# Optimization experiments

Hardware: AMD Instinct MI355X
Metric: run time of the kernel (lower is better)

The kernel has to match this reference:

```python
import jax, jax.numpy as jnp
import numpy as np

DIM = 64          # RefineNet dim
MDIM = 32         # EGNN m_dim
NLAY = 16         # 4 refine stages x n_layer=4 EGNN layers
VOCAB = 26        # len(RNAAlphabet)
PAD = 1           # padding_idx
NPOS = 4096 + PAD + 1
N = 23            # atoms per residue (hard-coded repeat(1,1,23))
EIN = 2 * DIM + 1 # edge MLP input dim

silu = jax.nn.silu

def _lin(x, w, b):
    return x @ w + b

def _egnn(feats, coors, p):
    ew1, eb1, ew2, eb2, cw1, cb1, cw2, cb2, nw1, nb1, nw2, nb2, g, beta = p
    B, Nn, D = feats.shape
    rel = coors[:, :, None, :] - coors[:, None, :, :]            # [B,Nn,Nn,3]
    dist = jnp.sum(rel * rel, -1, keepdims=True)                 # [B,Nn,Nn,1]
    fi = jnp.broadcast_to(feats[:, :, None, :], (B, Nn, Nn, D))
    fj = jnp.broadcast_to(feats[:, None, :, :], (B, Nn, Nn, D))
    edge_in = jnp.concatenate([fi, fj, dist], -1)                # [B,Nn,Nn,2D+1]
    m_ij = silu(_lin(silu(_lin(edge_in, ew1, eb1)), ew2, eb2))   # [B,Nn,Nn,MDIM]
    w = _lin(silu(_lin(m_ij, cw1, cb1)), cw2, cb2)[..., 0]       # [B,Nn,Nn]
    nrm = jnp.sqrt(dist)
    normed = rel / jnp.maximum(nrm, 1e-8)
    # CoorsNorm uses LayerNorm over a size-1 dim: (x - mean) == 0, so phase == beta
    phase = g * jnp.zeros_like(nrm) + beta
    coors_out = jnp.einsum('bij,bijc->bic', w * (1.0 / 50.0), phase * normed) + coors
    m_i = m_ij.sum(-2)
    node_out = _lin(silu(_lin(jnp.concatenate([feats, m_i], -1), nw1, nb1)), nw2, nb2) + feats
    return node_out, coors_out

def _forward(tokens, cords, tok_emb, pos_emb, ew1, eb1, ew2, eb2,
             cw1, cb1, cw2, cb2, nw1, nb1, nw2, nb2, ln_g, ln_b):
    stacked = (ew1, eb1, ew2, eb2, cw1, cb1, cw2, cb2, nw1, nb1, nw2, nb2, ln_g, ln_b)
    t = tokens[:, 0, :]                                  # [b,l]
    b, l = t.shape
    tok = jnp.broadcast_to(t[:, :, None], (b, l, N))     # repeat(1,1,23)
    fea = tok_emb[tok]                                   # [b,l,N,DIM]
    mask = (tok.reshape(b * l, N) != PAD).astype(jnp.int32)
    pos = jnp.cumsum(mask, axis=1) * mask + PAD
    fea = fea + pos_emb[pos].reshape(fea.shape)
    co = cords.reshape(b, l, N, 3)

    def run(f, c, start):
        for k in range(4):
            p = tuple(a[start + k] for a in stacked)
            f, c = _egnn(f, c, p)
        return f, c

    f, c = run(fea.reshape(b * l, N, DIM), co.reshape(b * l, N, 3), 0)
    f = jnp.swapaxes(f.reshape(b, l, N, DIM), 1, 2)
    c = jnp.swapaxes(c.reshape(b, l, N, 3), 1, 2)
    f, c = run(f.reshape(b * N, l, DIM), c.reshape(b * N, l, 3), 4)
    f = jnp.swapaxes(f.reshape(b, N, l, DIM), 1, 2)
    c = jnp.swapaxes(c.reshape(b, N, l, 3), 1, 2)
    f, c = run(f.reshape(b * l, N, DIM), c.reshape(b * l, N, 3), 8)
    f = jnp.swapaxes(f.reshape(b, l, N, DIM), 1, 2)
    c = jnp.swapaxes(c.reshape(b, l, N, 3), 1, 2)
    f, c = run(f.reshape(b * N, l, DIM), c.reshape(b * N, l, 3), 12)
    c = jnp.swapaxes(c.reshape(b, N, l, 3), 1, 2)
    return c.reshape(b, l * N, 3)

def setup_inputs():
    key = jax.random.key(0)
    ks = jax.random.split(key, 20)
    b, l = 2, 96
    s = 0.02
    def W(k, shp):
        return jax.random.normal(k, shp, jnp.float32) * s
    return {
        "tokens": jax.random.randint(ks[0], (b, 1, l), 0, VOCAB),
        "cords": jax.random.normal(ks[1], (b, l * N, 3), jnp.float32),
        "tok_emb": W(ks[2], (VOCAB, DIM)),
        "pos_emb": W(ks[3], (NPOS, DIM)).at[PAD].set(0.0),
        "ew1": W(ks[4], (NLAY, EIN, EIN * 2)), "eb1": W(ks[5], (NLAY, EIN * 2)),
        "ew2": W(ks[6], (NLAY, EIN * 2, MDIM)), "eb2": W(ks[7], (NLAY, MDIM)),
        "cw1": W(ks[8], (NLAY, MDIM, MDIM * 4)), "cb1": W(ks[9], (NLAY, MDIM * 4)),
        "cw2": W(ks[10], (NLAY, MDIM * 4, 1)), "cb2": W(ks[11], (NLAY, 1)),
        "nw1": W(ks[12], (NLAY, DIM + MDIM, DIM * 2)), "nb1": W(ks[13], (NLAY, DIM * 2)),
        "nw2": W(ks[14], (NLAY, DIM * 2, DIM)), "nb2": W(ks[15], (NLAY, DIM)),
        "ln_g": 1.0 + W(ks[16], (NLAY, 1)),
        "ln_b": W(ks[17], (NLAY, 1)),
    }

def reference(tokens, cords, tok_emb, pos_emb, ew1, eb1, ew2, eb2,
              cw1, cb1, cw2, cb2, nw1, nb1, nw2, nb2, ln_g, ln_b):
    return _forward(tokens, cords, tok_emb, pos_emb, ew1, eb1, ew2, eb2,
                    cw1, cb1, cw2, cb2, nw1, nb1, nw2, nb2, ln_g, ln_b)
```

## Files before the change

### kernel.cpp

```cpp
#include <hip/hip_runtime.h>
#include <math.h>

#define DIM   64
#define MDIM  32
#define NLAY  16
#define PAD   1
#define NB    2
#define LL    96
#define NN    23
#define NNODE (NB*LL*NN)
#define EIN   129
#define EH    258
#define KP    272
#define NK0   17
#define NH    128
#define BPITCH 276
#define APITCH 274
#define NOUT  516
#define NTILE 17
#define XP    104
#define HP    136
#define OP    560

typedef __attribute__((ext_vector_type(8)))  short        bf16x8;
typedef __attribute__((ext_vector_type(16))) float        f32x16;
typedef __attribute__((ext_vector_type(4)))  unsigned int uint4v;

__device__ __forceinline__ float silu_f(float x) {
    float e = __expf(-x);
    return x * __builtin_amdgcn_rcpf(1.0f + e);
}
__device__ __forceinline__ unsigned short bf16_rn(float x) {
    unsigned u = __float_as_uint(x);
    u += 0x7FFF + ((u >> 16) & 1);
    return (unsigned short)(u >> 16);
}
__device__ __forceinline__ float bf16_up(unsigned short h) {
    return __uint_as_float(((unsigned)h) << 16);
}
__device__ __forceinline__ int fwd_map(int nf, int alongL) {
    if (alongL) {
        int b = nf / (LL * NN);
        int rem = nf % (LL * NN);
        int l = rem / NN, n = rem % NN;
        return (b * NN + n) * LL + l;
    }
    return nf;
}
__device__ __forceinline__ int inv_map(int gnode, int alongL) {
    if (alongL) {
        int g = gnode / LL, l = gnode % LL;
        int b = g / NN, n = g % NN;
        return (b * LL + l) * NN + n;
    }
    return gnode;
}

__global__ void k_embed(const int* __restrict__ tokens,
                        const float* __restrict__ tok_emb,
                        const float* __restrict__ pos_emb,
                        float* __restrict__ feats) {
    int idx = blockIdx.x * blockDim.x + threadIdx.x;
    if (idx < NNODE * DIM) {
        int node = idx / DIM, d = idx % DIM;
        int b = node / (LL * NN);
        int rem = node % (LL * NN);
        int n = rem % NN;
        int l = rem / NN;
        int t = tokens[b * LL + l];
        float f = tok_emb[t * DIM + d];
        if (t != PAD) f += pos_emb[(n + 2) * DIM + d];
        feats[idx] = f;
    }
}

__global__ void k_prep(const float* __restrict__ ew1, const float* __restrict__ ew2,
                       const float* __restrict__ cw1, const float* __restrict__ cb1,
                       const float* __restrict__ cw2,
                       const float* __restrict__ nw1, const float* __restrict__ nw2,
                       float* __restrict__ wdF, unsigned short* __restrict__ ew2P,
                       unsigned short* __restrict__ cw1P,
                       float* __restrict__ cb1P, float* __restrict__ cw2P,
                       unsigned short* __restrict__ ew1P,
                       unsigned short* __restrict__ nw1P,
                       unsigned short* __restrict__ nw2P) {
    int idx = blockIdx.x * blockDim.x + threadIdx.x;
    if (idx < NLAY * KP) {
        int L = idx / KP, k = idx % KP;
        float v = (k < EH) ? ew1[(size_t)L * EIN * EH + 128 * EH + k] : 0.0f;
        wdF[idx] = bf16_up(bf16_rn(v));
    }
    if (idx < NLAY * NK0 * 512) {
        int L = idx / (NK0 * 512); int r = idx % (NK0 * 512);
        int k0 = r / 512; int r2 = r % 512;
        int lane = r2 >> 3, j = r2 & 7;
        int k = k0 * 16 + (lane >> 5) * 8 + j;
        int n = lane & 31;
        float v = (k < EH) ? ew2[((size_t)L * EH + k) * MDIM + n] : 0.0f;
        ew2P[idx] = bf16_rn(v);
    }
    if (idx < NLAY * 4096) {
        int L = idx / 4096; int r = idx % 4096;
        int mb = r / 1024; int r2 = r % 1024;
        int k0 = r2 / 512; int r3 = r2 % 512;
        int lane = r3 >> 3, j = r3 & 7;
        int k = k0 * 16 + (lane >> 5) * 8 + j;
        int o = mb * 32 + (lane & 31);
        cw1P[idx] = bf16_rn(cw1[((size_t)L * MDIM + k) * NH + o]);
    }
    if (idx < NLAY * 128) {
        int L = idx / 128; int r = idx % 128;
        int hlf = r / 64; int r2 = r % 64;
        int mb = r2 / 16, reg = r2 % 16;
        int o = mb * 32 + (reg & 3) + 8 * (reg >> 2) + 4 * hlf;
        cb1P[idx] = cb1[L * NH + o];
        cw2P[idx] = cw2[L * NH + o];
    }
    if (idx < NLAY * NTILE * 4 * 512) {
        int L = idx / (NTILE * 4 * 512); int r = idx % (NTILE * 4 * 512);
        int nt = r / 2048; int r2 = r % 2048;
        int ks = r2 / 512; int r3 = r2 % 512;
        int lane = r3 >> 3, j = r3 & 7;
        int d = ks * 16 + (lane >> 5) * 8 + j;
        int o = nt * 32 + (lane & 31);
        float v = 0.0f;
        if (o < EH)        v = ew1[(size_t)L * EIN * EH + d * EH + o];
        else if (o < NOUT) v = ew1[(size_t)L * EIN * EH + (DIM + d) * EH + (o - EH)];
        ew1P[idx] = bf16_rn(v);
    }
    if (idx < NLAY * 4 * 6 * 512) {
        int L = idx / 12288; int r = idx % 12288;
        int nt = r / 3072; int r2 = r % 3072;
        int ks = r2 / 512; int r3 = r2 % 512;
        int lane = r3 >> 3, j = r3 & 7;
        int k = ks * 16 + (lane >> 5) * 8 + j;
        int n = nt * 32 + (lane & 31);
        nw1P[idx] = bf16_rn(nw1[((size_t)L * (DIM + MDIM) + k) * NH + n]);
    }
    if (idx < NLAY * 2 * 8 * 512) {
        int L = idx / 8192; int r = idx % 8192;
        int nt = r / 4096; int r2 = r % 4096;
        int ks = r2 / 512; int r3 = r2 % 512;
        int lane = r3 >> 3, j = r3 & 7;
        int k = ks * 16 + (lane >> 5) * 8 + j;
        int n = nt * 32 + (lane & 31);
        nw2P[idx] = bf16_rn(nw2[((size_t)L * NH + k) * DIM + n]);
    }
}

__global__ __launch_bounds__(256)
void k_np(const float* __restrict__ fIn, const float* __restrict__ coSrc,
          const float* __restrict__ miL, const float* __restrict__ dL,
          const unsigned short* __restrict__ nw1PL, const float* __restrict__ nb1L,
          const unsigned short* __restrict__ nw2PL, const float* __restrict__ nb2L,
          const unsigned short* __restrict__ ew1PL, const float* __restrict__ eb1L,
          float* __restrict__ fOut, float* __restrict__ coDst,
          float* __restrict__ miNext, float* __restrict__ dNext,
          unsigned short* __restrict__ aH, unsigned short* __restrict__ bH,
          int aL0, int aL1, int doNode) {
    __shared__ unsigned short xS[32 * XP];
    __shared__ unsigned short hS[32 * HP];
    __shared__ unsigned short outS[32 * OP];
    __shared__ int gsrcS[32], gdstS[32];

    int n0  = blockIdx.x * 32;
    int tid = threadIdx.x;
    int wave = tid >> 6, lane = tid & 63, half = lane >> 5, e = lane & 31;

    if (tid < 32) {
        gsrcS[tid] = fwd_map(n0 + tid, aL0);
        gdstS[tid] = fwd_map(n0 + tid, aL1);
    }
    __syncthreads();

    for (int i = 0; i < 8; i++) {
        int x = tid + 256 * i;
        int node = x >> 6, d = x & 63;
        xS[node * XP + d] = bf16_rn(fIn[(n0 + node) * DIM + d]);
    }
    if (doNode) {
        for (int i = 0; i < 4; i++) {
            int x = tid + 256 * i;
            int node = x >> 5, d = x & 31;
            xS[node * XP + DIM + d] = bf16_rn(miL[(size_t)gsrcS[node] * MDIM + d]);
        }
    }
    for (int x = tid; x < 32 * 14; x += 256) {
        int node = x / 14, c = EH + x % 14;
        outS[node * OP + c] = 0;
    }
    if (tid < 96) {
        int node = tid / 3, c = tid % 3;
        int gs = gsrcS[node], gd = gdstS[node];
        float cv = coSrc[gs * 3 + c] + (doNode ? dL[gs * 3 + c] : 0.0f);
        coDst[gd * 3 + c] = cv;
        dNext[gd * 3 + c] = 0.0f;
    }
    for (int i = 0; i < 4; i++) {
        int x = tid + 256 * i;
        int node = x >> 5, d = x & 31;
        miNext[(size_t)gdstS[node] * MDIM + d] = 0.0f;
    }
    __syncthreads();

    if (doNode) {
        {
            int nt = wave;
            f32x16 acc;
#pragma unroll
            for (int q = 0; q < 16; q++) acc[q] = 0.0f;
#pragma unroll
            for (int ks = 0; ks < 6; ks++) {
                uint4v au = *(const uint4v*)(xS + e * XP + ks * 16 + half * 8);
                uint4v bu = *(const uint4v*)(nw1PL + ((size_t)(nt * 6 + ks) * 512 + lane * 8));
                acc = __builtin_amdgcn_mfma_f32_32x32x16_bf16(
                          __builtin_bit_cast(bf16x8, au),
                          __builtin_bit_cast(bf16x8, bu), acc, 0, 0, 0);
            }
            int o = nt * 32 + e;
            float b1 = nb1L[o];
#pragma unroll
            for (int q = 0; q < 16; q++) {
                int row = (q & 3) + 8 * (q >> 2) + 4 * half;
                hS[row * HP + o] = bf16_rn(silu_f(acc[q] + b1));
            }
        }
        __syncthreads();

        if (wave < 2) {
            int nt = wave;
            f32x16 acc;
#pragma unroll
            for (int q = 0; q < 16; q++) acc[q] = 0.0f;
#pragma unroll
            for (int ks = 0; ks < 8; ks++) {
                uint4v au = *(const uint4v*)(hS + e * HP + ks * 16 + half * 8);
                uint4v bu = *(const uint4v*)(nw2PL + ((size_t)(nt * 8 + ks) * 512 + lane * 8));
                acc = __builtin_amdgcn_mfma_f32_32x32x16_bf16(
                          __builtin_bit_cast(bf16x8, au),
                          __builtin_bit_cast(bf16x8, bu), acc, 0, 0, 0);
            }
            int o = nt * 32 + e;
            float b2 = nb2L[o];
#pragma unroll
            for (int q = 0; q < 16; q++) {
                int row = (q & 3) + 8 * (q >> 2) + 4 * half;
                float fo = acc[q] + b2 + bf16_up(xS[row * XP + o]);
                fOut[(size_t)(n0 + row) * DIM + o] = fo;
                xS[row * XP + o] = bf16_rn(fo);
            }
        }
        __syncthreads();
    }

    {
        uint4v afrag[4];
#pragma unroll
        for (int ks = 0; ks < 4; ks++)
            afrag[ks] = *(const uint4v*)(xS + e * XP + ks * 16 + half * 8);

        for (int nt = wave; nt < NTILE; nt += 4) {
            f32x16 acc;
#pragma unroll
            for (int q = 0; q < 16; q++) acc[q] = 0.0f;
#pragma unroll
            for (int ks = 0; ks < 4; ks++) {
                uint4v bu = *(const uint4v*)(ew1PL + ((size_t)(nt * 4 + ks) * 512 + lane * 8));
                acc = __builtin_amdgcn_mfma_f32_32x32x16_bf16(
                          __builtin_bit_cast(bf16x8, afrag[ks]),
                          __builtin_bit_cast(bf16x8, bu), acc, 0, 0, 0);
            }
            int o = nt * 32 + e;
            float eb = (o < EH) ? eb1L[o] : 0.0f;
            int col = (o < EH) ? o : (o + 14);
#pragma unroll
            for (int q = 0; q < 16; q++) {
                int row = (q & 3) + 8 * (q >> 2) + 4 * half;
                float v = (o < NOUT) ? (acc[q] + eb) : 0.0f;
                outS[row * OP + col] = bf16_rn(v);
            }
        }
    }
    __syncthreads();

    for (int x = tid; x < 32 * 68; x += 256) {
        int row = x / 68, off = x % 68;
        int gd = gdstS[row];
        uint4v v = *(const uint4v*)(outS + row * OP + off * 8);
        if (off < 34) *(uint4v*)(aH + (size_t)gd * KP + off * 8) = v;
        else          *(uint4v*)(bH + (size_t)gd * KP + (off - 34) * 8) = v;
    }
}

__global__ __launch_bounds__(256, 3)
void k_edge(const unsigned short* __restrict__ aH,
            const unsigned short* __restrict__ bH,
            const float* __restrict__ coorsO,
            const float* __restrict__ wdFL,
            const unsigned short* __restrict__ ew2PL,
            const float* __restrict__ eb2L,
            const unsigned short* __restrict__ cw1PL,
            const float* __restrict__ cb1PL,
            const float* __restrict__ cw2PL,
            const float* __restrict__ cb2L,
            const float* __restrict__ lnbL,
            float* __restrict__ miBuf, float* __restrict__ deltaBuf,
            int Nn, int itpg, int njt) {
    __shared__ unsigned short bS[32 * BPITCH];
    __shared__ float          aSf[8 * APITCH];
    __shared__ float          wdS[KP];
    __shared__ float          cjS[32 * 3];
    __shared__ float          cbS[128], cwS[128];
    __shared__ unsigned short mT[4][32 * 36];

    int bid = blockIdx.x;
    int g   = bid / (itpg * njt);
    int r   = bid % (itpg * njt);
    int it  = r / njt;
    int jt  = r % njt;

    int tid  = threadIdx.x;
    int wave = tid >> 6, lane = tid & 63, half = lane >> 5, e = lane & 31;

    int j0  = jt * 32;
    int njr = Nn - j0; if (njr > 32) njr = 32;
    int i0  = it * 8;
    int nir = Nn - i0; if (nir > 8) nir = 8;

    {
        const unsigned int* src = (const unsigned int*)(bH + (size_t)(g * Nn + j0) * KP);
        unsigned int* dst = (unsigned int*)bS;
        int tot = njr * 136;
        for (int x = tid; x < tot; x += 256) {
            int rr = x / 136, c = x % 136;
            dst[rr * (BPITCH / 2) + c] = src[rr * 136 + c];
        }
        const unsigned short* asrc = aH + (size_t)(g * Nn + i0) * KP;
        int at = nir * KP;
        for (int x = tid; x < at; x += 256) {
            int rr = x / KP, k = x % KP;
            aSf[rr * APITCH + k] = bf16_up(asrc[rr * KP + k]);
        }
        for (int x = tid; x < KP; x += 256) wdS[x] = wdFL[x];
        if (tid < njr * 3) cjS[tid] = coorsO[(g * Nn + j0) * 3 + tid];
        if (tid < 128) { cbS[tid] = cb1PL[tid]; cwS[tid] = cw2PL[tid]; }
    }
    __syncthreads();

    float eb2v = eb2L[e];
    float beta = lnbL[0];
    float cb2v = cb2L[0];

    int  jc     = (e < njr) ? e : (njr - 1);
    bool jvalid = (e < njr);
    float cjx = cjS[jc * 3 + 0], cjy = cjS[jc * 3 + 1], cjz = cjS[jc * 3 + 2];

    unsigned short* mW = &mT[wave][0];
    const unsigned short* bRow = bS + jc * BPITCH;

    for (int s = 0; s < 2; s++) {
        int il = wave * 2 + s;
        if (il >= nir) break;
        int i  = i0 + il;
        int gi = g * Nn + i;

        float cix = coorsO[gi * 3 + 0], ciy = coorsO[gi * 3 + 1], ciz = coorsO[gi * 3 + 2];
        float rx = cix - cjx, ry = ciy - cjy, rz = ciz - cjz;
        float dist = rx * rx + ry * ry + rz * rz;

        const float* aRowF = aSf + il * APITCH;

        f32x16 acc;
#pragma unroll
        for (int q = 0; q < 16; q++) acc[q] = 0.0f;

#pragma unroll
        for (int k0 = 0; k0 < NK0; k0++) {
            int ko = k0 * 16 + half * 8;
            uint2 b01 = *(const uint2*)(bRow + ko);
            uint2 b23 = *(const uint2*)(bRow + ko + 4);
            uint4v eu = *(const uint4v*)(ew2PL + ((size_t)k0 * 64 + lane) * 8);
            unsigned bw[4] = {b01.x, b01.y, b23.x, b23.y};
            uint4v hu;
#pragma unroll
            for (int p = 0; p < 4; p++) {
                float2 av = *(const float2*)(aRowF + ko + 2 * p);
                float2 wv = *(const float2*)(wdS + ko + 2 * p);
                float bL = __uint_as_float(bw[p] << 16);
                float bU = __uint_as_float(bw[p] & 0xFFFF0000u);
                float hL = silu_f(av.x + bL + dist * wv.x);
                float hU = silu_f(av.y + bU + dist * wv.y);
                hu[p] = __builtin_amdgcn_perm(__float_as_uint(hU), __float_as_uint(hL),
                                              0x07060302u);
            }
            acc = __builtin_amdgcn_mfma_f32_32x32x16_bf16(
                      __builtin_bit_cast(bf16x8, hu),
                      __builtin_bit_cast(bf16x8, eu), acc, 0, 0, 0);
        }

        float miAcc = 0.0f;
        float mv[16];
#pragma unroll
        for (int q = 0; q < 16; q++) {
            int row = (q & 3) + 8 * (q >> 2) + 4 * half;
            float m = silu_f(acc[q] + eb2v);
            m = (j0 + row < Nn) ? m : 0.0f;
            mv[q] = m;
            miAcc += m;
        }
#pragma unroll
        for (int q = 0; q < 4; q++) {
            unsigned lo = __builtin_amdgcn_perm(__float_as_uint(mv[q * 4 + 1]),
                                                __float_as_uint(mv[q * 4 + 0]), 0x07060302u);
            unsigned hi = __builtin_amdgcn_perm(__float_as_uint(mv[q * 4 + 3]),
                                                __float_as_uint(mv[q * 4 + 2]), 0x07060302u);
            int row0 = 8 * q + 4 * half;
            *(uint2*)&mW[e * 36 + row0] = make_uint2(lo, hi);
        }

        miAcc += __shfl_xor(miAcc, 32, 64);
        if (half == 0) atomicAdd(&miBuf[gi * MDIM + e], miAcc);

        bf16x8 bq[2];
#pragma unroll
        for (int k0 = 0; k0 < 2; k0++) {
            uint4v t;
#pragma unroll
            for (int p = 0; p < 4; p++) {
                unsigned v0 = mW[(k0 * 16 + half * 8 + 2 * p    ) * 36 + e];
                unsigned v1 = mW[(k0 * 16 + half * 8 + 2 * p + 1) * 36 + e];
                t[p] = v0 | (v1 << 16);
            }
            bq[k0] = __builtin_bit_cast(bf16x8, t);
        }

        float wAcc = 0.0f;
#pragma unroll
        for (int mb = 0; mb < 4; mb++) {
            f32x16 sacc;
#pragma unroll
            for (int q = 0; q < 16; q++) sacc[q] = 0.0f;
#pragma unroll
            for (int k0 = 0; k0 < 2; k0++) {
                uint4v cu = *(const uint4v*)(cw1PL + ((size_t)(mb * 2 + k0) * 64 + lane) * 8);
                sacc = __builtin_amdgcn_mfma_f32_32x32x16_bf16(
                           __builtin_bit_cast(bf16x8, cu), bq[k0], sacc, 0, 0, 0);
            }
            const float* cb1q = cbS + (half * 4 + mb) * 16;
            const float* cw2q = cwS + (half * 4 + mb) * 16;
#pragma unroll
            for (int q = 0; q < 16; q++) {
                wAcc += silu_f(sacc[q] + cb1q[q]) * cw2q[q];
            }
        }
        wAcc += __shfl_xor(wAcc, 32, 64);
        float w = wAcc + cb2v;
        float nrm = sqrtf(dist);
        float scale = (w * 0.02f) * beta * __builtin_amdgcn_rcpf(fmaxf(nrm, 1e-8f));

        float dAx = 0.0f, dAy = 0.0f, dAz = 0.0f;
        if (jvalid && half == 0) {
            dAx = scale * rx; dAy = scale * ry; dAz = scale * rz;
        }
#pragma unroll
        for (int m = 16; m >= 1; m >>= 1) {
            dAx += __shfl_xor(dAx, m, 64);
            dAy += __shfl_xor(dAy, m, 64);
            dAz += __shfl_xor(dAz, m, 64);
        }
        if (lane == 0) {
            atomicAdd(&deltaBuf[gi * 3 + 0], dAx);
            atomicAdd(&deltaBuf[gi * 3 + 1], dAy);
            atomicAdd(&deltaBuf[gi * 3 + 2], dAz);
        }
    }
}

__global__ void k_fin(const float* __restrict__ co, const float* __restrict__ dl,
                      float* __restrict__ out) {
    int idx = blockIdx.x * blockDim.x + threadIdx.x;
    if (idx < NNODE * 3) {
        int gnode = idx / 3, c = idx % 3;
        int nf = inv_map(gnode, 1);
        out[nf * 3 + c] = co[idx] + dl[idx];
    }
}

extern "C" void kernel_launch(void* const* d_in, const int* in_sizes, int n_in,
                              void* d_out, int out_size, void* d_ws, size_t ws_size,
                              hipStream_t stream) {
    (void)in_sizes; (void)n_in; (void)out_size; (void)ws_size;

    const int*   tokens  = (const int*)d_in[0];
    const float* cords   = (const float*)d_in[1];
    const float* tok_emb = (const float*)d_in[2];
    const float* pos_emb = (const float*)d_in[3];
    const float* ew1 = (const float*)d_in[4];
    const float* eb1 = (const float*)d_in[5];
    const float* ew2 = (const float*)d_in[6];
    const float* eb2 = (const float*)d_in[7];
    const float* cw1 = (const float*)d_in[8];
    const float* cb1 = (const float*)d_in[9];
    const float* cw2 = (const float*)d_in[10];
    const float* cb2 = (const float*)d_in[11];
    const float* nw1 = (const float*)d_in[12];
    const float* nb1 = (const float*)d_in[13];
    const float* nw2 = (const float*)d_in[14];
    const float* nb2 = (const float*)d_in[15];
    const float* lnb = (const float*)d_in[17];

    float* wf = (float*)d_ws;
    float* featsA = wf; wf += NNODE * DIM;
    float* featsB = wf; wf += NNODE * DIM;
    float* coorsO0 = wf; wf += NNODE * 3;
    float* coorsO1 = wf; wf += NNODE * 3;
    float* mi0  = wf; wf += NNODE * MDIM;
    float* mi1  = wf; wf += NNODE * MDIM;
    float* dl0  = wf; wf += NNODE * 3;
    float* dl1  = wf; wf += NNODE * 3;
    float* cb1P = wf; wf += NLAY * 128;
    float* cw2P = wf; wf += NLAY * 128;
    float* wdF  = wf; wf += NLAY * KP;

    uintptr_t p = (uintptr_t)wf; p = (p + 15) & ~(uintptr_t)15;
    unsigned short* wh = (unsigned short*)p;
    unsigned short* aHb  = wh; wh += (size_t)NNODE * KP;
    unsigned short* bHb  = wh; wh += (size_t)NNODE * KP;
    unsigned short* ew2P = wh; wh += NLAY * NK0 * 512;
    unsigned short* cw1P = wh; wh += NLAY * 4096;
    unsigned short* ew1P = wh; wh += (size_t)NLAY * NTILE * 4 * 512;
    unsigned short* nw1P = wh; wh += (size_t)NLAY * 4 * 6 * 512;
    unsigned short* nw2P = wh; wh += (size_t)NLAY * 2 * 8 * 512;

    float* coorsO[2] = {coorsO0, coorsO1};
    float* miB[2]    = {mi0, mi1};
    float* dlB[2]    = {dl0, dl1};

    int prepN = NLAY * NTILE * 4 * 512;
    k_prep<<<(prepN + 255) / 256, 256, 0, stream>>>(
        ew1, ew2, cw1, cb1, cw2, nw1, nw2,
        wdF, ew2P, cw1P, cb1P, cw2P, ew1P, nw1P, nw2P);
    k_embed<<<(NNODE * DIM + 255) / 256, 256, 0, stream>>>(
        tokens, tok_emb, pos_emb, featsA);

    float* fCur = featsA; float* fNxt = featsB;

    k_np<<<NNODE / 32, 256, 0, stream>>>(
        fCur, cords, nullptr, nullptr,
        nullptr, nullptr, nullptr, nullptr,
        ew1P + 0, eb1 + 0,
        fNxt, coorsO[0], miB[0], dlB[0],
        aHb, bHb, 0, 0, 0);

    for (int L = 0; L < NLAY; L++) {
        int alongL = (L / 4) % 2;
        int idx  = L & 1;
        int Nn   = alongL ? LL : NN;
        int njt  = alongL ? 3 : 1;
        int itpg = (Nn + 7) / 8;
        int groups = NNODE / Nn;

        k_edge<<<groups * itpg * njt, 256, 0, stream>>>(
            aHb, bHb, coorsO[idx],
            wdF + L * KP, ew2P + (size_t)L * NK0 * 512, eb2 + L * MDIM,
            cw1P + (size_t)L * 4096, cb1P + L * 128, cw2P + L * 128,
            cb2 + L, lnb + L, miB[idx], dlB[idx], Nn, itpg, njt);

        if (L < NLAY - 1) {
            int aL1 = ((L + 1) / 4) % 2;
            int nidx = (L + 1) & 1;
            k_np<<<NNODE / 32, 256, 0, stream>>>(
                fCur, coorsO[idx], miB[idx], dlB[idx],
                nw1P + (size_t)L * 4 * 6 * 512, nb1 + L * NH,
                nw2P + (size_t)L * 2 * 8 * 512, nb2 + L * DIM,
                ew1P + (size_t)(L + 1) * NTILE * 4 * 512, eb1 + (size_t)(L + 1) * EH,
                fNxt, coorsO[nidx], miB[nidx], dlB[nidx],
                aHb, bHb, alongL, aL1, 1);
            float* t = fCur; fCur = fNxt; fNxt = t;
        } else {
            k_fin<<<(NNODE * 3 + 255) / 256, 256, 0, stream>>>(
                coorsO[idx], dlB[idx], (float*)d_out);
        }
    }
}
```

Before: 1.055 ms.

## Interleave two edge rows per wave in k_edge with packed float2 SiLU math

Restructures k_edge so each wave computes the first edge-MLP GEMM for both of its i rows in one k-loop, reusing the B-row, wd and ew2 fragment loads across two MFMA accumulators. The SiLU and bias math is rewritten on float2 vectors (exp2/rcp) to allow packed FP32 instructions, and cb1/cw2 are interleaved into one buffer so a single vector load serves both. The A pitch is padded for 16-byte aligned vector reads, and a fast path skips the row masking when the j tile is full. Holding two accumulators raises register pressure, which may hurt occupancy under the 3-blocks-per-SM launch bound.

```diff
diff --git a/kernel.cpp b/kernel.cpp
--- a/kernel.cpp
+++ b/kernel.cpp
@@ -15,7 +15,7 @@
 #define NK0   17
 #define NH    128
 #define BPITCH 276
-#define APITCH 274
+#define APITCH 276
 #define NOUT  516
 #define NTILE 17
 #define XP    104
@@ -25,10 +25,25 @@
 typedef __attribute__((ext_vector_type(8)))  short        bf16x8;
 typedef __attribute__((ext_vector_type(16))) float        f32x16;
 typedef __attribute__((ext_vector_type(4)))  unsigned int uint4v;
+typedef __attribute__((ext_vector_type(2)))  float        f32x2;
+typedef __attribute__((ext_vector_type(4)))  float        f32x4;
+
+__device__ __forceinline__ f32x2 mk2(float a, float b) { f32x2 r; r.x = a; r.y = b; return r; }
 
 __device__ __forceinline__ float silu_f(float x) {
     float e = __expf(-x);
     return x * __builtin_amdgcn_rcpf(1.0f + e);
+}
+__device__ __forceinline__ f32x2 silu2(f32x2 x) {
+    f32x2 t = x * (-1.44269504f);
+    f32x2 e;
+    e.x = __builtin_amdgcn_exp2f(t.x);
+    e.y = __builtin_amdgcn_exp2f(t.y);
+    f32x2 den = e + 1.0f;
+    f32x2 r;
+    r.x = __builtin_amdgcn_rcpf(den.x);
+    r.y = __builtin_amdgcn_rcpf(den.y);
+    return x * r;
 }
 __device__ __forceinline__ unsigned short bf16_rn(float x) {
     unsigned u = __float_as_uint(x);
@@ -37,6 +52,15 @@
 }
 __device__ __forceinline__ float bf16_up(unsigned short h) {
     return __uint_as_float(((unsigned)h) << 16);
+}
+__device__ __forceinline__ f32x2 ub2(unsigned bw) {
+    return mk2(__uint_as_float(bw << 16), __uint_as_float(bw & 0xFFFF0000u));
+}
+__device__ __forceinline__ unsigned hpack(f32x2 a2, f32x2 w2, f32x2 b2, f32x2 d2) {
+    f32x2 x2 = a2 + b2;
+    x2 = __builtin_elementwise_fma(d2, w2, x2);
+    f32x2 h2 = silu2(x2);
+    return __builtin_amdgcn_perm(__float_as_uint(h2.y), __float_as_uint(h2.x), 0x07060302u);
 }
 __device__ __forceinline__ int fwd_map(int nf, int alongL) {
     if (alongL) {
@@ -80,7 +104,7 @@
                        const float* __restrict__ nw1, const float* __restrict__ nw2,
                        float* __restrict__ wdF, unsigned short* __restrict__ ew2P,
                        unsigned short* __restrict__ cw1P,
-                       float* __restrict__ cb1P, float* __restrict__ cw2P,
+                       float* __restrict__ cbwP,
                        unsigned short* __restrict__ ew1P,
                        unsigned short* __restrict__ nw1P,
                        unsigned short* __restrict__ nw2P) {
@@ -113,8 +137,8 @@
         int hlf = r / 64; int r2 = r % 64;
         int mb = r2 / 16, reg = r2 % 16;
         int o = mb * 32 + (reg & 3) + 8 * (reg >> 2) + 4 * hlf;
-        cb1P[idx] = cb1[L * NH + o];
-        cw2P[idx] = cw2[L * NH + o];
+        cbwP[(size_t)L * 256 + r * 2 + 0] = cb1[L * NH + o];
+        cbwP[(size_t)L * 256 + r * 2 + 1] = cw2[L * NH + o];
     }
     if (idx < NLAY * NTILE * 4 * 512) {
         int L = idx / (NTILE * 4 * 512); int r = idx % (NTILE * 4 * 512);
@@ -300,17 +324,16 @@
             const unsigned short* __restrict__ ew2PL,
             const float* __restrict__ eb2L,
             const unsigned short* __restrict__ cw1PL,
-            const float* __restrict__ cb1PL,
-            const float* __restrict__ cw2PL,
+            const float* __restrict__ cbwPL,
             const float* __restrict__ cb2L,
             const float* __restrict__ lnbL,
             float* __restrict__ miBuf, float* __restrict__ deltaBuf,
             int Nn, int itpg, int njt) {
     __shared__ unsigned short bS[32 * BPITCH];
-    __shared__ float          aSf[8 * APITCH];
-    __shared__ float          wdS[KP];
-    __shared__ float          cjS[32 * 3];
-    __shared__ float          cbS[128], cwS[128];
+    __shared__ __align__(16) float aSf[8 * APITCH];
+    __shared__ __align__(16) float wdS[KP];
+    __shared__ float cjS[32 * 3];
+    __shared__ __align__(16) float cbwS[256];
     __shared__ unsigned short mT[4][32 * 36];
 
     int bid = blockIdx.x;
@@ -343,7 +366,7 @@
         }
         for (int x = tid; x < KP; x += 256) wdS[x] = wdFL[x];
         if (tid < njr * 3) cjS[tid] = coorsO[(g * Nn + j0) * 3 + tid];
-        if (tid < 128) { cbS[tid] = cb1PL[tid]; cwS[tid] = cw2PL[tid]; }
+        if (tid < 256) cbwS[tid] = cbwPL[tid];
     }
     __syncthreads();
 
@@ -358,56 +381,96 @@
     unsigned short* mW = &mT[wave][0];
     const unsigned short* bRow = bS + jc * BPITCH;
 
+    int il0 = wave * 2, il1 = wave * 2 + 1;
+    bool v0 = il0 < nir, v1 = il1 < nir;
+    int gi0 = g * Nn + i0 + (v0 ? il0 : 0);
+    int gi1 = g * Nn + i0 + (v1 ? il1 : 0);
+
+    float rx0, ry0, rz0, d0, rx1, ry1, rz1, d1;
+    {
+        float cx = coorsO[gi0 * 3 + 0], cy = coorsO[gi0 * 3 + 1], cz = coorsO[gi0 * 3 + 2];
+        rx0 = cx - cjx; ry0 = cy - cjy; rz0 = cz - cjz;
+        d0 = rx0 * rx0 + ry0 * ry0 + rz0 * rz0;
+        cx = coorsO[gi1 * 3 + 0]; cy = coorsO[gi1 * 3 + 1]; cz = coorsO[gi1 * 3 + 2];
+        rx1 = cx - cjx; ry1 = cy - cjy; rz1 = cz - cjz;
+        d1 = rx1 * rx1 + ry1 * ry1 + rz1 * rz1;
+    }
+    f32x2 d20 = mk2(d0, d0), d21 = mk2(d1, d1);
+    const float* aR0 = aSf + (v0 ? il0 : 0) * APITCH;
+    const float* aR1 = aSf + (v1 ? il1 : 0) * APITCH;
+
+    f32x16 acc0, acc1;
+#pragma unroll
+    for (int q = 0; q < 16; q++) { acc0[q] = 0.0f; acc1[q] = 0.0f; }
+
+#pragma unroll
+    for (int k0 = 0; k0 < NK0; k0++) {
+        int ko = k0 * 16 + half * 8;
+        uint2 bA = *(const uint2*)(bRow + ko);
+        uint2 bB = *(const uint2*)(bRow + ko + 4);
+        f32x4 wv0 = *(const f32x4*)(wdS + ko);
+        f32x4 wv1 = *(const f32x4*)(wdS + ko + 4);
+        uint4v eu = *(const uint4v*)(ew2PL + ((size_t)k0 * 64 + lane) * 8);
+        f32x2 b2_0 = ub2(bA.x), b2_1 = ub2(bA.y), b2_2 = ub2(bB.x), b2_3 = ub2(bB.y);
+
+        f32x4 a00 = *(const f32x4*)(aR0 + ko);
+        f32x4 a01 = *(const f32x4*)(aR0 + ko + 4);
+        uint4v hu0;
+        hu0[0] = hpack(a00.xy, wv0.xy, b2_0, d20);
+        hu0[1] = hpack(a00.zw, wv0.zw, b2_1, d20);
+        hu0[2] = hpack(a01.xy, wv1.xy, b2_2, d20);
+        hu0[3] = hpack(a01.zw, wv1.zw, b2_3, d20);
+        acc0 = __builtin_amdgcn_mfma_f32_32x32x16_bf16(
+                   __builtin_bit_cast(bf16x8, hu0),
+                   __builtin_bit_cast(bf16x8, eu), acc0, 0, 0, 0);
+
+        f32x4 a10 = *(const f32x4*)(aR1 + ko);
+        f32x4 a11 = *(const f32x4*)(aR1 + ko + 4);
+        uint4v hu1;
+        hu1[0] = hpack(a10.xy, wv0.xy, b2_0, d21);
+        hu1[1] = hpack(a10.zw, wv0.zw, b2_1, d21);
+        hu1[2] = hpack(a11.xy, wv1.xy, b2_2, d21);
+        hu1[3] = hpack(a11.zw, wv1.zw, b2_3, d21);
+        acc1 = __builtin_amdgcn_mfma_f32_32x32x16_bf16(
+                   __builtin_bit_cast(bf16x8, hu1),
+                   __builtin_bit_cast(bf16x8, eu), acc1, 0, 0, 0);
+    }
+
+    f32x2 ebp = mk2(eb2v, eb2v);
+
+#pragma unroll
     for (int s = 0; s < 2; s++) {
-        int il = wave * 2 + s;
-        if (il >= nir) break;
-        int i  = i0 + il;
-        int gi = g * Nn + i;
-
-        float cix = coorsO[gi * 3 + 0], ciy = coorsO[gi * 3 + 1], ciz = coorsO[gi * 3 + 2];
-        float rx = cix - cjx, ry = ciy - cjy, rz = ciz - cjz;
-        float dist = rx * rx + ry * ry + rz * rz;
-
-        const float* aRowF = aSf + il * APITCH;
-
-        f32x16 acc;
-#pragma unroll
-        for (int q = 0; q < 16; q++) acc[q] = 0.0f;
-
-#pragma unroll
-        for (int k0 = 0; k0 < NK0; k0++) {
-            int ko = k0 * 16 + half * 8;
-            uint2 b01 = *(const uint2*)(bRow + ko);
-            uint2 b23 = *(const uint2*)(bRow + ko + 4);
-            uint4v eu = *(const uint4v*)(ew2PL + ((size_t)k0 * 64 + lane) * 8);
-            unsigned bw[4] = {b01.x, b01.y, b23.x, b23.y};
-            uint4v hu;
-#pragma unroll
-            for (int p = 0; p < 4; p++) {
-                float2 av = *(const float2*)(aRowF + ko + 2 * p);
-                float2 wv = *(const float2*)(wdS + ko + 2 * p);
-                float bL = __uint_as_float(bw[p] << 16);
-                float bU = __uint_as_float(bw[p] & 0xFFFF0000u);
-                float hL = silu_f(av.x + bL + dist * wv.x);
-                float hU = silu_f(av.y + bU + dist * wv.y);
-                hu[p] = __builtin_amdgcn_perm(__float_as_uint(hU), __float_as_uint(hL),
-                                              0x07060302u);
-            }
-            acc = __builtin_amdgcn_mfma_f32_32x32x16_bf16(
-                      __builtin_bit_cast(bf16x8, hu),
-                      __builtin_bit_cast(bf16x8, eu), acc, 0, 0, 0);
-        }
-
-        float miAcc = 0.0f;
+        if (!(s ? v1 : v0)) continue;
+        int gi = s ? gi1 : gi0;
+        float rx = s ? rx1 : rx0, ry = s ? ry1 : ry0, rz = s ? rz1 : rz0;
+        float dist = s ? d1 : d0;
+
         float mv[16];
-#pragma unroll
-        for (int q = 0; q < 16; q++) {
-            int row = (q & 3) + 8 * (q >> 2) + 4 * half;
-            float m = silu_f(acc[q] + eb2v);
-            m = (j0 + row < Nn) ? m : 0.0f;
-            mv[q] = m;
-            miAcc += m;
-        }
+        f32x2 mi2 = mk2(0.0f, 0.0f);
+        if (njr == 32) {
+#pragma unroll
+            for (int qp = 0; qp < 8; qp++) {
+                int q = qp * 2;
+                f32x2 x2 = mk2(s ? acc1[q] : acc0[q], s ? acc1[q + 1] : acc0[q + 1]) + ebp;
+                f32x2 m2 = silu2(x2);
+                mv[q] = m2.x; mv[q + 1] = m2.y;
+                mi2 += m2;
+            }
+        } else {
+#pragma unroll
+            for (int qp = 0; qp < 8; qp++) {
+                int q = qp * 2;
+                f32x2 x2 = mk2(s ? acc1[q] : acc0[q], s ? acc1[q + 1] : acc0[q + 1]) + ebp;
+                f32x2 m2 = silu2(x2);
+                int row0 = (q & 3) + 8 * (q >> 2) + 4 * half;
+                if (j0 + row0 >= Nn) m2.x = 0.0f;
+                if (j0 + row0 + 1 >= Nn) m2.y = 0.0f;
+                mv[q] = m2.x; mv[q + 1] = m2.y;
+                mi2 += m2;
+            }
+        }
+        float miAcc = mi2.x + mi2.y;
+
 #pragma unroll
         for (int q = 0; q < 4; q++) {
             unsigned lo = __builtin_amdgcn_perm(__float_as_uint(mv[q * 4 + 1]),
@@ -427,14 +490,14 @@
             uint4v t;
 #pragma unroll
             for (int p = 0; p < 4; p++) {
-                unsigned v0 = mW[(k0 * 16 + half * 8 + 2 * p    ) * 36 + e];
-                unsigned v1 = mW[(k0 * 16 + half * 8 + 2 * p + 1) * 36 + e];
-                t[p] = v0 | (v1 << 16);
+                unsigned w0 = mW[(k0 * 16 + half * 8 + 2 * p    ) * 36 + e];
+                unsigned w1 = mW[(k0 * 16 + half * 8 + 2 * p + 1) * 36 + e];
+                t[p] = w0 | (w1 << 16);
             }
             bq[k0] = __builtin_bit_cast(bf16x8, t);
         }
 
-        float wAcc = 0.0f;
+        f32x2 w2a = mk2(0.0f, 0.0f);
 #pragma unroll
         for (int mb = 0; mb < 4; mb++) {
             f32x16 sacc;
@@ -446,13 +509,16 @@
                 sacc = __builtin_amdgcn_mfma_f32_32x32x16_bf16(
                            __builtin_bit_cast(bf16x8, cu), bq[k0], sacc, 0, 0, 0);
             }
-            const float* cb1q = cbS + (half * 4 + mb) * 16;
-            const float* cw2q = cwS + (half * 4 + mb) * 16;
-#pragma unroll
-            for (int q = 0; q < 16; q++) {
-                wAcc += silu_f(sacc[q] + cb1q[q]) * cw2q[q];
-            }
-        }
+            const f32x4* cv = (const f32x4*)(cbwS + (half * 4 + mb) * 32);
+#pragma unroll
+            for (int qp = 0; qp < 8; qp++) {
+                f32x4 c4 = cv[qp];
+                f32x2 s2 = mk2(sacc[2 * qp], sacc[2 * qp + 1]) + mk2(c4.x, c4.z);
+                f32x2 p2 = silu2(s2);
+                w2a = __builtin_elementwise_fma(p2, mk2(c4.y, c4.w), w2a);
+            }
+        }
+        float wAcc = w2a.x + w2a.y;
         wAcc += __shfl_xor(wAcc, 32, 64);
         float w = wAcc + cb2v;
         float nrm = sqrtf(dist);
@@ -518,8 +584,7 @@
     float* mi1  = wf; wf += NNODE * MDIM;
     float* dl0  = wf; wf += NNODE * 3;
     float* dl1  = wf; wf += NNODE * 3;
-    float* cb1P = wf; wf += NLAY * 128;
-    float* cw2P = wf; wf += NLAY * 128;
+    float* cbwP = wf; wf += NLAY * 256;
     float* wdF  = wf; wf += NLAY * KP;
 
     uintptr_t p = (uintptr_t)wf; p = (p + 15) & ~(uintptr_t)15;
@@ -539,7 +604,7 @@
     int prepN = NLAY * NTILE * 4 * 512;
     k_prep<<<(prepN + 255) / 256, 256, 0, stream>>>(
         ew1, ew2, cw1, cb1, cw2, nw1, nw2,
-        wdF, ew2P, cw1P, cb1P, cw2P, ew1P, nw1P, nw2P);
+        wdF, ew2P, cw1P, cbwP, ew1P, nw1P, nw2P);
     k_embed<<<(NNODE * DIM + 255) / 256, 256, 0, stream>>>(
         tokens, tok_emb, pos_emb, featsA);
 
@@ -563,7 +628,7 @@
         k_edge<<<groups * itpg * njt, 256, 0, stream>>>(
             aHb, bHb, coorsO[idx],
             wdF + L * KP, ew2P + (size_t)L * NK0 * 512, eb2 + L * MDIM,
-            cw1P + (size_t)L * 4096, cb1P + L * 128, cw2P + L * 128,
+            cw1P + (size_t)L * 4096, cbwP + (size_t)L * 256,
             cb2 + L, lnb + L, miB[idx], dlB[idx], Nn, itpg, njt);
 
         if (L < NLAY - 1) {
```

New measurement: 972.0 us. -7.9%, faster.
